# Kernel tuning notes

Hardware: AMD Instinct MI355X
Metric: run time of the kernel (lower is better)

The kernel has to match this reference:

```python
import jax, jax.numpy as jnp
import numpy as np

H = 2048
W = 2048
N = H * W
NUM_CC = 1 << 20
N_ITERS = 20  # pointer-doubling covers tree depth up to 2**20 (actual depth ~ e*ln N ~ 45)
EPS = 1e-10


def _log_scaling(f):
    # f: [NUM_CC, 15] = xmin, ymin, xmax, ymax, area, angle, pca_big, pca_small, hu1..hu7
    # -> [NUM_CC, 17] = xmin..ymax, log(area), signed-log(pca_big, pca_small, hu1..hu7), lshape, cos(angle), sin(angle)
    lshape = jnp.sqrt(f[:, 7:8]) / (jnp.sqrt(f[:, 6:7]) + EPS)
    cosangle = jnp.cos(f[:, 5:6])
    sinangle = jnp.sin(f[:, 5:6])
    log_area = jnp.log(f[:, 4:5])
    signed_log = jnp.log(jnp.abs(f[:, 6:]) + EPS) * jnp.sign(f[:, 6:])
    return jnp.concatenate([f[:, :4], log_area, signed_log, lshape, cosangle, sinangle], axis=1)


def _tree_path_sum(contrib, parent):
    # out[p] = sum of contrib over p and all its ancestors (root has parent == -1).
    # Parallel pointer-doubling: after k steps acc[i] sums contrib over 2**k chain nodes.
    acc, par = contrib, parent
    for _ in range(N_ITERS):
        valid = par >= 0
        pidx = jnp.where(valid, par, 0)
        acc = acc + jnp.where(valid, acc[pidx], jnp.zeros((), acc.dtype))
        par = jnp.where(valid, par[pidx], -1)
    return acc


def setup_inputs() -> dict:
    rng = np.random.default_rng(0)
    # random recursive tree: parent[i] uniform in [0, i), root = node 0
    parent = (rng.random(N) * np.arange(N)).astype(np.int32)
    parent[0] = -1
    cc_id = rng.integers(0, NUM_CC, size=N).astype(np.int32)
    diff = rng.standard_normal(N).astype(np.float32)
    attrs = np.empty((NUM_CC, 15), np.float32)
    attrs[:, :4] = rng.random((NUM_CC, 4)) * 100.0          # bbox coords
    attrs[:, 4] = rng.random(NUM_CC) * 1000.0 + 1.0         # area (>0 for log)
    attrs[:, 5] = rng.standard_normal(NUM_CC)               # angle
    attrs[:, 6:8] = rng.random((NUM_CC, 2)) + 0.01          # pca_big/pca_small (>=0 for sqrt)
    attrs[:, 8:] = rng.standard_normal((NUM_CC, 7)).astype(np.float32)  # hu moments
    weight = ((rng.random((17, 1)) - 0.5) * 0.02).astype(np.float32)
    bias = np.zeros((1,), np.float32)
    return {
        "diff": jnp.asarray(diff),
        "attributes": jnp.asarray(attrs),
        "weight": jnp.asarray(weight),
        "bias": jnp.asarray(bias),
        "parent": jnp.asarray(parent),
        "cc_id": jnp.asarray(cc_id),
    }


def reference(diff, attributes, weight, bias, parent, cc_id):
    rescaled = _log_scaling(attributes)                                   # [NUM_CC, 17]
    cc_scores = jax.nn.sigmoid(rescaled @ weight + bias[None, :])[:, 0]   # [NUM_CC]
    contrib = diff * cc_scores[cc_id]                                     # [N]
    out = _tree_path_sum(contrib, parent)                                 # [N]
    return out.reshape(H, W)
```

## Files before the change

kernel.cpp:

```cpp
#include <hip/hip_runtime.h>

#define EPSF 1e-10f

struct alignas(8) Node { int par; float c; };

__device__ __forceinline__ float signed_log(float x) {
    float sg = (x > 0.f) ? 1.f : ((x < 0.f) ? -1.f : 0.f);
    return logf(fabsf(x) + EPSF) * sg;
}

__global__ void scores_kernel(const float* __restrict__ attrs,
                              const float* __restrict__ weight,
                              const float* __restrict__ bias,
                              float* __restrict__ scores, int num_cc) {
    int i = blockIdx.x * blockDim.x + threadIdx.x;
    if (i >= num_cc) return;
    const float* f = attrs + (long long)i * 15;
    float w[17];
#pragma unroll
    for (int k = 0; k < 17; ++k) w[k] = weight[k];
    float acc = bias[0];
    acc += w[0] * f[0] + w[1] * f[1] + w[2] * f[2] + w[3] * f[3];
    acc += w[4] * logf(f[4]);
#pragma unroll
    for (int j = 0; j < 9; ++j) acc += w[5 + j] * signed_log(f[6 + j]);
    float lshape = sqrtf(f[7]) / (sqrtf(f[6]) + EPSF);
    acc += w[14] * lshape;
    acc += w[15] * cosf(f[5]);
    acc += w[16] * sinf(f[5]);
    scores[i] = 1.f / (1.f + expf(-acc));
}

__global__ void pack_kernel(const float* __restrict__ diff,
                            const int* __restrict__ parent,
                            const int* __restrict__ cc_id,
                            const float* __restrict__ scores,
                            Node* __restrict__ packed, int n) {
    int i = blockIdx.x * blockDim.x + threadIdx.x;
    if (i >= n) return;
    Node nd;
    nd.par = parent[i];
    nd.c = diff[i] * scores[cc_id[i]];
    packed[i] = nd;
}

__global__ void contrib_kernel(const float* __restrict__ diff,
                               const int* __restrict__ cc_id,
                               const float* __restrict__ scores,
                               float* __restrict__ contrib, int n) {
    int i = blockIdx.x * blockDim.x + threadIdx.x;
    if (i >= n) return;
    contrib[i] = diff[i] * scores[cc_id[i]];
}

__global__ void walk_base(const Node* __restrict__ packed,
                          float* __restrict__ out, int range_end) {
    int i = blockIdx.x * blockDim.x + threadIdx.x;
    if (i >= range_end) return;
    float s = 0.f;
    int cur = i;
    while (cur >= 0) {
        Node nd = packed[cur];
        s += nd.c;
        cur = nd.par;
    }
    out[i] = s;
}

__global__ void walk_phase(const Node* __restrict__ packed,
                           float* __restrict__ out, int lo, int hi) {
    int i = lo + blockIdx.x * blockDim.x + threadIdx.x;
    if (i >= hi) return;
    float s = 0.f;
    int cur = i;
    while (cur >= lo) {
        Node nd = packed[cur];
        s += nd.c;
        cur = nd.par;
    }
    s += out[cur];
    out[i] = s;
}

__global__ void walk_base2(const int* __restrict__ parent,
                           const float* __restrict__ contrib,
                           float* __restrict__ out, int range_end) {
    int i = blockIdx.x * blockDim.x + threadIdx.x;
    if (i >= range_end) return;
    float s = 0.f;
    int cur = i;
    while (cur >= 0) {
        s += contrib[cur];
        cur = parent[cur];
    }
    out[i] = s;
}

__global__ void walk_phase2(const int* __restrict__ parent,
                            const float* __restrict__ contrib,
                            float* __restrict__ out, int lo, int hi) {
    int i = lo + blockIdx.x * blockDim.x + threadIdx.x;
    if (i >= hi) return;
    float s = 0.f;
    int cur = i;
    while (cur >= lo) {
        s += contrib[cur];
        cur = parent[cur];
    }
    s += out[cur];
    out[i] = s;
}

static inline int iminh(int a, int b) { return a < b ? a : b; }

extern "C" void kernel_launch(void* const* d_in, const int* in_sizes, int n_in,
                              void* d_out, int out_size, void* d_ws, size_t ws_size,
                              hipStream_t stream) {
    const float* diff   = (const float*)d_in[0];
    const float* attrs  = (const float*)d_in[1];
    const float* weight = (const float*)d_in[2];
    const float* bias   = (const float*)d_in[3];
    const int*   parent = (const int*)d_in[4];
    const int*   cc_id  = (const int*)d_in[5];
    float* out = (float*)d_out;

    const int n      = in_sizes[0];
    const int num_cc = in_sizes[1] / 15;

    float* scores = (float*)d_ws;
    const size_t scores_bytes = (size_t)num_cc * sizeof(float);
    const size_t packed_need  = scores_bytes + (size_t)n * sizeof(Node);
    const bool use_packed = ws_size >= packed_need;

    const int TB = 256;
    scores_kernel<<<(num_cc + TB - 1) / TB, TB, 0, stream>>>(attrs, weight, bias, scores, num_cc);

    const int B = 65536;
    if (use_packed) {
        Node* packed = (Node*)((char*)d_ws + scores_bytes);
        pack_kernel<<<(n + TB - 1) / TB, TB, 0, stream>>>(diff, parent, cc_id, scores, packed, n);
        int base_end = iminh(B, n);
        walk_base<<<(base_end + TB - 1) / TB, TB, 0, stream>>>(packed, out, base_end);
        int lo = base_end;
        while (lo < n) {
            long long hi_ll = (long long)lo * 4;
            int hi = (hi_ll > n) ? n : (int)hi_ll;
            walk_phase<<<((hi - lo) + TB - 1) / TB, TB, 0, stream>>>(packed, out, lo, hi);
            lo = hi;
        }
    } else {
        float* contrib = (float*)((char*)d_ws + scores_bytes);
        contrib_kernel<<<(n + TB - 1) / TB, TB, 0, stream>>>(diff, cc_id, scores, contrib, n);
        int base_end = iminh(B, n);
        walk_base2<<<(base_end + TB - 1) / TB, TB, 0, stream>>>(parent, contrib, out, base_end);
        int lo = base_end;
        while (lo < n) {
            long long hi_ll = (long long)lo * 4;
            int hi = (hi_ll > n) ? n : (int)hi_ll;
            walk_phase2<<<((hi - lo) + TB - 1) / TB, TB, 0, stream>>>(parent, contrib, out, lo, hi);
            lo = hi;
        }
    }
}
```

Before: 141.1 us.

## Vectorize pack kernel, add nontemporal loads/stores, retune phase boundaries

Result: faster. 130.5 us (-7.5%).

```diff
diff --git a/kernel.cpp b/kernel.cpp
--- a/kernel.cpp
+++ b/kernel.cpp
@@ -3,6 +3,9 @@
 #define EPSF 1e-10f
 
 struct alignas(8) Node { int par; float c; };
+
+typedef int   v4i __attribute__((ext_vector_type(4)));
+typedef float v4f __attribute__((ext_vector_type(4)));
 
 __device__ __forceinline__ float signed_log(float x) {
     float sg = (x > 0.f) ? 1.f : ((x < 0.f) ? -1.f : 0.f);
@@ -28,15 +31,35 @@
     acc += w[14] * lshape;
     acc += w[15] * cosf(f[5]);
     acc += w[16] * sinf(f[5]);
-    scores[i] = 1.f / (1.f + expf(-acc));
+    __builtin_nontemporal_store(1.f / (1.f + expf(-acc)), &scores[i]);
+}
+
+__global__ void pack_kernel4(const v4f* __restrict__ diff4,
+                             const v4i* __restrict__ parent4,
+                             const v4i* __restrict__ cc4,
+                             const float* __restrict__ scores,
+                             v4i* __restrict__ packed2, int n4) {
+    int i = blockIdx.x * blockDim.x + threadIdx.x;
+    if (i >= n4) return;
+    v4f d = __builtin_nontemporal_load(&diff4[i]);
+    v4i p = __builtin_nontemporal_load(&parent4[i]);
+    v4i c = __builtin_nontemporal_load(&cc4[i]);
+    float s0 = scores[c.x], s1 = scores[c.y], s2 = scores[c.z], s3 = scores[c.w];
+    v4i o0, o1;
+    o0.x = p.x; o0.y = __float_as_int(d.x * s0);
+    o0.z = p.y; o0.w = __float_as_int(d.y * s1);
+    o1.x = p.z; o1.y = __float_as_int(d.z * s2);
+    o1.z = p.w; o1.w = __float_as_int(d.w * s3);
+    __builtin_nontemporal_store(o0, &packed2[2 * i]);
+    __builtin_nontemporal_store(o1, &packed2[2 * i + 1]);
 }
 
 __global__ void pack_kernel(const float* __restrict__ diff,
                             const int* __restrict__ parent,
                             const int* __restrict__ cc_id,
                             const float* __restrict__ scores,
-                            Node* __restrict__ packed, int n) {
-    int i = blockIdx.x * blockDim.x + threadIdx.x;
+                            Node* __restrict__ packed, int lo, int n) {
+    int i = lo + blockIdx.x * blockDim.x + threadIdx.x;
     if (i >= n) return;
     Node nd;
     nd.par = parent[i];
@@ -44,42 +67,39 @@
     packed[i] = nd;
 }
 
-__global__ void contrib_kernel(const float* __restrict__ diff,
-                               const int* __restrict__ cc_id,
-                               const float* __restrict__ scores,
-                               float* __restrict__ contrib, int n) {
-    int i = blockIdx.x * blockDim.x + threadIdx.x;
-    if (i >= n) return;
-    contrib[i] = diff[i] * scores[cc_id[i]];
+__device__ __forceinline__ void load_self_nt(const Node* p, int i, int& par, float& c) {
+    long long raw = __builtin_nontemporal_load((const long long*)(p + i));
+    par = (int)(raw & 0xffffffffLL);
+    c = __int_as_float((int)(raw >> 32));
 }
 
 __global__ void walk_base(const Node* __restrict__ packed,
                           float* __restrict__ out, int range_end) {
     int i = blockIdx.x * blockDim.x + threadIdx.x;
     if (i >= range_end) return;
-    float s = 0.f;
-    int cur = i;
+    int cur; float s;
+    load_self_nt(packed, i, cur, s);
     while (cur >= 0) {
         Node nd = packed[cur];
         s += nd.c;
         cur = nd.par;
     }
-    out[i] = s;
+    __builtin_nontemporal_store(s, &out[i]);
 }
 
 __global__ void walk_phase(const Node* __restrict__ packed,
                            float* __restrict__ out, int lo, int hi) {
     int i = lo + blockIdx.x * blockDim.x + threadIdx.x;
     if (i >= hi) return;
-    float s = 0.f;
-    int cur = i;
+    int cur; float s;
+    load_self_nt(packed, i, cur, s);
     while (cur >= lo) {
         Node nd = packed[cur];
         s += nd.c;
         cur = nd.par;
     }
     s += out[cur];
-    out[i] = s;
+    __builtin_nontemporal_store(s, &out[i]);
 }
 
 __global__ void walk_base2(const int* __restrict__ parent,
@@ -89,10 +109,7 @@
     if (i >= range_end) return;
     float s = 0.f;
     int cur = i;
-    while (cur >= 0) {
-        s += contrib[cur];
-        cur = parent[cur];
-    }
+    while (cur >= 0) { s += contrib[cur]; cur = parent[cur]; }
     out[i] = s;
 }
 
@@ -103,12 +120,18 @@
     if (i >= hi) return;
     float s = 0.f;
     int cur = i;
-    while (cur >= lo) {
-        s += contrib[cur];
-        cur = parent[cur];
-    }
+    while (cur >= lo) { s += contrib[cur]; cur = parent[cur]; }
     s += out[cur];
     out[i] = s;
+}
+
+__global__ void contrib_kernel(const float* __restrict__ diff,
+                               const int* __restrict__ cc_id,
+                               const float* __restrict__ scores,
+                               float* __restrict__ contrib, int n) {
+    int i = blockIdx.x * blockDim.x + threadIdx.x;
+    if (i >= n) return;
+    contrib[i] = diff[i] * scores[cc_id[i]];
 }
 
 static inline int iminh(int a, int b) { return a < b ? a : b; }
@@ -135,15 +158,23 @@
     const int TB = 256;
     scores_kernel<<<(num_cc + TB - 1) / TB, TB, 0, stream>>>(attrs, weight, bias, scores, num_cc);
 
-    const int B = 65536;
+    const int BASE   = 131072;
+    const int R2_MIN = 1 << 19;
+
     if (use_packed) {
         Node* packed = (Node*)((char*)d_ws + scores_bytes);
-        pack_kernel<<<(n + TB - 1) / TB, TB, 0, stream>>>(diff, parent, cc_id, scores, packed, n);
-        int base_end = iminh(B, n);
+        if ((n & 3) == 0) {
+            pack_kernel4<<<(n / 4 + TB - 1) / TB, TB, 0, stream>>>(
+                (const v4f*)diff, (const v4i*)parent, (const v4i*)cc_id, scores, (v4i*)packed, n / 4);
+        } else {
+            pack_kernel<<<(n + TB - 1) / TB, TB, 0, stream>>>(diff, parent, cc_id, scores, packed, 0, n);
+        }
+        int base_end = iminh(BASE, n);
         walk_base<<<(base_end + TB - 1) / TB, TB, 0, stream>>>(packed, out, base_end);
         int lo = base_end;
         while (lo < n) {
-            long long hi_ll = (long long)lo * 4;
+            int ratio = (lo < R2_MIN) ? 4 : 2;
+            long long hi_ll = (long long)lo * ratio;
             int hi = (hi_ll > n) ? n : (int)hi_ll;
             walk_phase<<<((hi - lo) + TB - 1) / TB, TB, 0, stream>>>(packed, out, lo, hi);
             lo = hi;
@@ -151,11 +182,12 @@
     } else {
         float* contrib = (float*)((char*)d_ws + scores_bytes);
         contrib_kernel<<<(n + TB - 1) / TB, TB, 0, stream>>>(diff, cc_id, scores, contrib, n);
-        int base_end = iminh(B, n);
+        int base_end = iminh(BASE, n);
         walk_base2<<<(base_end + TB - 1) / TB, TB, 0, stream>>>(parent, contrib, out, base_end);
         int lo = base_end;
         while (lo < n) {
-            long long hi_ll = (long long)lo * 4;
+            int ratio = (lo < R2_MIN) ? 4 : 2;
+            long long hi_ll = (long long)lo * ratio;
             int hi = (hi_ll > n) ? n : (int)hi_ll;
             walk_phase2<<<((hi - lo) + TB - 1) / TB, TB, 0, stream>>>(parent, contrib, out, lo, hi);
             lo = hi;
```
